# Kernel optimization log

Measured on AMD Instinct MI355X. Metric: run time of the kernel, lower is better.

Reference implementation:

```python
import jax, jax.numpy as jnp
import numpy as np

B, D, N = 256, 256, 100000
NUM_CLUSTERS, NUM_CLASSES = 100, 1000


def setup_inputs() -> dict:
    key = jax.random.key(0)
    k1, k2, k3, k4, k5, k6 = jax.random.split(key, 6)
    return {
        "feature": jax.random.normal(k1, (B, D), dtype=jnp.float32),
        "feature_bank": jax.random.normal(k2, (N, D), dtype=jnp.float32),
        "cluster_label_bank": jax.random.randint(k3, (N,), 0, NUM_CLUSTERS, dtype=jnp.int64)
            if jax.config.jax_enable_x64 else jax.random.randint(k3, (N,), 0, NUM_CLUSTERS).astype(jnp.int32),
        "class_label_bank": jax.random.randint(k4, (N,), 0, NUM_CLASSES).astype(jnp.int32),
        "cluster_idx": jax.random.randint(k5, (B,), 0, NUM_CLUSTERS).astype(jnp.int32),
        "gt_label": jax.random.randint(k6, (B,), 0, NUM_CLASSES).astype(jnp.int32),
    }


def reference(feature, feature_bank, cluster_label_bank, class_label_bank, cluster_idx, gt_label):
    # Masks: primary = same cluster AND different class; fallback = different class only.
    cluster_label_bank = cluster_label_bank.astype(jnp.int32)
    same_cluster = cluster_label_bank[None, :] == cluster_idx[:, None].astype(jnp.int32)  # [B, N]
    diff_class = class_label_bank[None, :] != gt_label[:, None]                            # [B, N]
    mask_primary = same_cluster & diff_class
    has_primary = mask_primary.any(axis=1, keepdims=True)
    mask = jnp.where(has_primary, mask_primary, diff_class)  # [B, N]

    # Euclidean distances (torch.cdist p=2): ||a-b|| via expanded squared form.
    a2 = jnp.sum(feature * feature, axis=1)[:, None]              # [B, 1]
    b2 = jnp.sum(feature_bank * feature_bank, axis=1)[None, :]    # [1, N]
    d2 = a2 + b2 - 2.0 * (feature @ feature_bank.T)               # [B, N]
    dist = jnp.sqrt(jnp.maximum(d2, 0.0))

    # Masked argmin over the bank, then gather negatives.
    dist_masked = jnp.where(mask, dist, jnp.inf)
    neg_idx = jnp.argmin(dist_masked, axis=1)                     # [B]
    negatives = feature_bank[neg_idx]                             # [B, D]
    return negatives
```

## Files before the change

### kernel.cpp

```cpp
#include <hip/hip_runtime.h>
#include <climits>

typedef __attribute__((ext_vector_type(8))) short s8;
typedef __attribute__((ext_vector_type(4))) float f32x4;

#define BQ    256
#define DDIM  256
#define NBANK 100000
#define BN    64
#define NJB   ((NBANK + BN - 1) / BN)
#define SENT  1e30f

__device__ inline void splitElem(float x, s8& h, s8& l, int i) {
    unsigned u  = __float_as_uint(x);
    unsigned uh = (u + 0x8000u) & 0xFFFF0000u;
    h[i] = (short)(uh >> 16);
    float lf = x - __uint_as_float(uh);
    l[i] = (short)((__float_as_uint(lf) + 0x8000u) >> 16);
}

__device__ inline void split8(const float4 v0, const float4 v1, s8& h, s8& l) {
    splitElem(v0.x, h, l, 0); splitElem(v0.y, h, l, 1);
    splitElem(v0.z, h, l, 2); splitElem(v0.w, h, l, 3);
    splitElem(v1.x, h, l, 4); splitElem(v1.y, h, l, 5);
    splitElem(v1.z, h, l, 6); splitElem(v1.w, h, l, 7);
}

__device__ inline float sq8(const float4 v0, const float4 v1, float s) {
    s = fmaf(v0.x, v0.x, s); s = fmaf(v0.y, v0.y, s);
    s = fmaf(v0.z, v0.z, s); s = fmaf(v0.w, v0.w, s);
    s = fmaf(v1.x, v1.x, s); s = fmaf(v1.y, v1.y, s);
    s = fmaf(v1.z, v1.z, s); s = fmaf(v1.w, v1.w, s);
    return s;
}

__global__ __launch_bounds__(512) void split_feature(
    const float* __restrict__ feature, s8* __restrict__ fH, s8* __restrict__ fL)
{
    const int t    = blockIdx.x * 512 + threadIdx.x;
    const int lane = t & 63, ks = (t >> 6) & 7, rt = t >> 9;
    const int row  = rt * 16 + (lane & 15);
    const int k0   = ks * 32 + (lane >> 4) * 8;
    const float* p = feature + (size_t)row * DDIM + k0;
    const float4 v0 = *(const float4*)p;
    const float4 v1 = *(const float4*)(p + 4);
    s8 h, l;
    split8(v0, v1, h, l);
    fH[t] = h; fL[t] = l;
}

__global__ __launch_bounds__(256, 3) void gemm_argmin_partial(
    const s8* __restrict__ fH, const s8* __restrict__ fL,
    const float* __restrict__ bank,
    const int* __restrict__ cluster_label, const int* __restrict__ class_label,
    const int* __restrict__ cluster_idx,  const int* __restrict__ gt_label,
    float* __restrict__ wsPV, int* __restrict__ wsPI,
    float* __restrict__ wsDV, int* __restrict__ wsDI)
{
    __shared__ __align__(16) s8 bHs[4 * 64];
    __shared__ __align__(16) s8 bLs[4 * 64];
    __shared__ float b2s[BN];
    __shared__ int clsS[BN], cluS[BN], rowGt[BQ], rowClu[BQ];

    const int tid = threadIdx.x;
    const int jb  = blockIdx.x;
    const int j0  = jb * BN;

    if (tid < BN) {
        int jg = j0 + tid;
        int jc = jg < NBANK ? jg : NBANK - 1;
        clsS[tid] = class_label[jc];
        cluS[tid] = cluster_label[jc];
    }
    rowGt[tid]  = gt_label[tid];
    rowClu[tid] = cluster_idx[tid];

    const int col = tid >> 2, q = tid & 3;
    const int ct_s = col >> 4, cl_s = col & 15;
    const int wi   = ct_s * 64 + q * 16 + cl_s;
    {
        int jcol = j0 + col;
        jcol = jcol < NBANK ? jcol : NBANK - 1;
        const float* gb = bank + (size_t)jcol * DDIM + q * 8;

        const int w = tid >> 6, lane = tid & 63;
        const int g = lane >> 4, c = lane & 15;

        f32x4 acc[4][4];
        #pragma unroll
        for (int ct = 0; ct < 4; ++ct)
            #pragma unroll
            for (int rt = 0; rt < 4; ++rt)
                acc[ct][rt] = (f32x4){0.f, 0.f, 0.f, 0.f};
        float sqa = 0.f;

        float4 cur0 = *(const float4*)(gb);
        float4 cur1 = *(const float4*)(gb + 4);

        for (int s = 0; s < 8; ++s) {
            s8 aHr[4], aLr[4];
            #pragma unroll
            for (int rt = 0; rt < 4; ++rt) {
                const int RT = w * 4 + rt;
                aHr[rt] = fH[(RT * 8 + s) * 64 + lane];
                aLr[rt] = fL[(RT * 8 + s) * 64 + lane];
            }
            __syncthreads();
            {
                s8 h, l;
                split8(cur0, cur1, h, l);
                sqa = sq8(cur0, cur1, sqa);
                bHs[wi] = h;
                bLs[wi] = l;
            }
            __syncthreads();
            if (s < 7) {
                cur0 = *(const float4*)(gb + (s + 1) * 32);
                cur1 = *(const float4*)(gb + (s + 1) * 32 + 4);
            }
            #pragma unroll
            for (int ct = 0; ct < 4; ++ct) {
                const s8 bh = bHs[ct * 64 + lane];
                const s8 bl = bLs[ct * 64 + lane];
                #pragma unroll
                for (int rt = 0; rt < 4; ++rt) {
                    acc[ct][rt] = __builtin_amdgcn_mfma_f32_16x16x32_bf16(aHr[rt], bh, acc[ct][rt], 0, 0, 0);
                    acc[ct][rt] = __builtin_amdgcn_mfma_f32_16x16x32_bf16(aHr[rt], bl, acc[ct][rt], 0, 0, 0);
                    acc[ct][rt] = __builtin_amdgcn_mfma_f32_16x16x32_bf16(aLr[rt], bh, acc[ct][rt], 0, 0, 0);
                    acc[ct][rt] = __builtin_amdgcn_mfma_f32_16x16x32_bf16(aLr[rt], bl, acc[ct][rt], 0, 0, 0);
                }
            }
        }

        sqa += __shfl_xor(sqa, 1);
        sqa += __shfl_xor(sqa, 2);
        if (q == 0) b2s[col] = sqa;
        __syncthreads();

        #pragma unroll
        for (int rt = 0; rt < 4; ++rt) {
            #pragma unroll
            for (int r = 0; r < 4; ++r) {
                const int row  = w * 64 + rt * 16 + g * 4 + r;
                const int myGt = rowGt[row], myClu = rowClu[row];
                float bpv = SENT, bdv = SENT;
                int   bpi = INT_MAX, bdi = INT_MAX;
                #pragma unroll
                for (int ct = 0; ct < 4; ++ct) {
                    const int jg = j0 + ct * 16 + c;
                    const float sc = b2s[ct * 16 + c] - 2.f * acc[ct][rt][r];
                    if (jg < NBANK && clsS[ct * 16 + c] != myGt) {
                        if (sc < bdv) { bdv = sc; bdi = jg; }
                        if (cluS[ct * 16 + c] == myClu && sc < bpv) { bpv = sc; bpi = jg; }
                    }
                }
                #pragma unroll
                for (int off = 1; off < 16; off <<= 1) {
                    float vv = __shfl_xor(bpv, off); int ii = __shfl_xor(bpi, off);
                    if (vv < bpv || (vv == bpv && ii < bpi)) { bpv = vv; bpi = ii; }
                    vv = __shfl_xor(bdv, off); ii = __shfl_xor(bdi, off);
                    if (vv < bdv || (vv == bdv && ii < bdi)) { bdv = vv; bdi = ii; }
                }
                if (c == 0) {
                    const size_t o = (size_t)row * NJB + jb;
                    wsPV[o] = bpv; wsPI[o] = bpi;
                    wsDV[o] = bdv; wsDI[o] = bdi;
                }
            }
        }
    }
}

__global__ __launch_bounds__(256) void reduce_gather(
    const float* __restrict__ wsPV, const int* __restrict__ wsPI,
    const float* __restrict__ wsDV, const int* __restrict__ wsDI,
    const float* __restrict__ bank, float* __restrict__ out)
{
    const int row = blockIdx.x, tid = threadIdx.x;
    float bpv = SENT, bdv = SENT;
    int   bpi = INT_MAX, bdi = INT_MAX;
    for (int b = tid; b < NJB; b += 256) {
        float v = wsPV[(size_t)row * NJB + b]; int ix = wsPI[(size_t)row * NJB + b];
        if (v < bpv || (v == bpv && ix < bpi)) { bpv = v; bpi = ix; }
        v = wsDV[(size_t)row * NJB + b]; ix = wsDI[(size_t)row * NJB + b];
        if (v < bdv || (v == bdv && ix < bdi)) { bdv = v; bdi = ix; }
    }
    #pragma unroll
    for (int off = 32; off > 0; off >>= 1) {
        float v = __shfl_down(bpv, off); int ix = __shfl_down(bpi, off);
        if (v < bpv || (v == bpv && ix < bpi)) { bpv = v; bpi = ix; }
        v = __shfl_down(bdv, off); ix = __shfl_down(bdi, off);
        if (v < bdv || (v == bdv && ix < bdi)) { bdv = v; bdi = ix; }
    }
    __shared__ float swPV[4], swDV[4];
    __shared__ int   swPI[4], swDI[4];
    __shared__ int   sIdx;
    const int lane = tid & 63, wv = tid >> 6;
    if (lane == 0) { swPV[wv] = bpv; swPI[wv] = bpi; swDV[wv] = bdv; swDI[wv] = bdi; }
    __syncthreads();
    if (tid == 0) {
        float pv = swPV[0]; int pi = swPI[0];
        float dv = swDV[0]; int di = swDI[0];
        #pragma unroll
        for (int w = 1; w < 4; ++w) {
            if (swPV[w] < pv || (swPV[w] == pv && swPI[w] < pi)) { pv = swPV[w]; pi = swPI[w]; }
            if (swDV[w] < dv || (swDV[w] == dv && swDI[w] < di)) { dv = swDV[w]; di = swDI[w]; }
        }
        sIdx = (pi != INT_MAX) ? pi : ((di != INT_MAX) ? di : 0);
    }
    __syncthreads();
    out[row * DDIM + tid] = bank[(size_t)sIdx * DDIM + tid];
}

extern "C" void kernel_launch(void* const* d_in, const int* in_sizes, int n_in,
                              void* d_out, int out_size, void* d_ws, size_t ws_size,
                              hipStream_t stream) {
    const float* feature       = (const float*)d_in[0];
    const float* bank          = (const float*)d_in[1];
    const int*   cluster_label = (const int*)d_in[2];
    const int*   class_label   = (const int*)d_in[3];
    const int*   cluster_idx   = (const int*)d_in[4];
    const int*   gt_label      = (const int*)d_in[5];
    float* out = (float*)d_out;

    s8* fH = (s8*)d_ws;
    s8* fL = fH + 8192;
    float* base = (float*)((char*)d_ws + 2 * 8192 * sizeof(s8));
    const size_t per = (size_t)BQ * NJB;
    float* wsPV = base;
    int*   wsPI = (int*)base + per;
    float* wsDV = base + 2 * per;
    int*   wsDI = (int*)base + 3 * per;

    hipLaunchKernelGGL(split_feature, dim3(16), dim3(512), 0, stream, feature, fH, fL);
    hipLaunchKernelGGL(gemm_argmin_partial, dim3(NJB), dim3(256), 0, stream,
                       fH, fL, bank, cluster_label, class_label, cluster_idx, gt_label,
                       wsPV, wsPI, wsDV, wsDI);
    hipLaunchKernelGGL(reduce_gather, dim3(BQ), dim3(256), 0, stream,
                       wsPV, wsPI, wsDV, wsDI, bank, out);
}
```

Before: 244.7 us.

## Stage full-K bank tile in shared memory and transpose partial workspace layout

Each block now loads its whole 64x256 bank tile into registers up front, splits it into bf16 hi/lo parts and writes them all to shared memory, then runs the full K loop of MFMAs with no per-step barriers. This removes the 16 __syncthreads of the old software-pipelined loop and lets all global loads be in flight at once. The partial-result workspace is transposed to block-major so the per-block stores are contiguous and the reduction reads are strided. Occupancy hint drops from 3 to 2 blocks per CU and shared memory grows to 64KB, which may reduce latency hiding.

```diff
diff --git a/kernel.cpp b/kernel.cpp
--- a/kernel.cpp
+++ b/kernel.cpp
@@ -49,7 +49,7 @@
     fH[t] = h; fL[t] = l;
 }
 
-__global__ __launch_bounds__(256, 3) void gemm_argmin_partial(
+__global__ __launch_bounds__(256, 2) void gemm_argmin_fullk(
     const s8* __restrict__ fH, const s8* __restrict__ fL,
     const float* __restrict__ bank,
     const int* __restrict__ cluster_label, const int* __restrict__ class_label,
@@ -57,8 +57,8 @@
     float* __restrict__ wsPV, int* __restrict__ wsPI,
     float* __restrict__ wsDV, int* __restrict__ wsDI)
 {
-    __shared__ __align__(16) s8 bHs[4 * 64];
-    __shared__ __align__(16) s8 bLs[4 * 64];
+    __shared__ __align__(16) s8 bHs[8 * 4 * 64];
+    __shared__ __align__(16) s8 bLs[8 * 4 * 64];
     __shared__ float b2s[BN];
     __shared__ int clsS[BN], cluS[BN], rowGt[BQ], rowClu[BQ];
 
@@ -77,95 +77,91 @@
 
     const int col = tid >> 2, q = tid & 3;
     const int ct_s = col >> 4, cl_s = col & 15;
-    const int wi   = ct_s * 64 + q * 16 + cl_s;
-    {
-        int jcol = j0 + col;
-        jcol = jcol < NBANK ? jcol : NBANK - 1;
-        const float* gb = bank + (size_t)jcol * DDIM + q * 8;
-
-        const int w = tid >> 6, lane = tid & 63;
-        const int g = lane >> 4, c = lane & 15;
-
-        f32x4 acc[4][4];
-        #pragma unroll
-        for (int ct = 0; ct < 4; ++ct)
-            #pragma unroll
-            for (int rt = 0; rt < 4; ++rt)
-                acc[ct][rt] = (f32x4){0.f, 0.f, 0.f, 0.f};
-        float sqa = 0.f;
-
-        float4 cur0 = *(const float4*)(gb);
-        float4 cur1 = *(const float4*)(gb + 4);
-
-        for (int s = 0; s < 8; ++s) {
-            s8 aHr[4], aLr[4];
+    int jcol = j0 + col; jcol = jcol < NBANK ? jcol : NBANK - 1;
+    const float* gb = bank + (size_t)jcol * DDIM + q * 8;
+
+    float4 v0[8], v1[8];
+    #pragma unroll
+    for (int s = 0; s < 8; ++s) {
+        v0[s] = *(const float4*)(gb + s * 32);
+        v1[s] = *(const float4*)(gb + s * 32 + 4);
+    }
+    float sqa = 0.f;
+    #pragma unroll
+    for (int s = 0; s < 8; ++s) {
+        s8 h, l;
+        split8(v0[s], v1[s], h, l);
+        sqa = sq8(v0[s], v1[s], sqa);
+        const int wi = (s * 4 + ct_s) * 64 + q * 16 + cl_s;
+        bHs[wi] = h;
+        bLs[wi] = l;
+    }
+    sqa += __shfl_xor(sqa, 1);
+    sqa += __shfl_xor(sqa, 2);
+    if (q == 0) b2s[col] = sqa;
+    __syncthreads();
+
+    const int w = tid >> 6, lane = tid & 63;
+    const int g = lane >> 4, c = lane & 15;
+
+    f32x4 acc[4][4];
+    #pragma unroll
+    for (int ct = 0; ct < 4; ++ct)
+        #pragma unroll
+        for (int rt = 0; rt < 4; ++rt)
+            acc[ct][rt] = (f32x4){0.f, 0.f, 0.f, 0.f};
+
+    #pragma unroll
+    for (int s = 0; s < 8; ++s) {
+        s8 aH[4], aL[4];
+        #pragma unroll
+        for (int rt = 0; rt < 4; ++rt) {
+            const int RT = w * 4 + rt;
+            aH[rt] = fH[(RT * 8 + s) * 64 + lane];
+            aL[rt] = fL[(RT * 8 + s) * 64 + lane];
+        }
+        #pragma unroll
+        for (int ct = 0; ct < 4; ++ct) {
+            const s8 bh = bHs[(s * 4 + ct) * 64 + lane];
+            const s8 bl = bLs[(s * 4 + ct) * 64 + lane];
             #pragma unroll
             for (int rt = 0; rt < 4; ++rt) {
-                const int RT = w * 4 + rt;
-                aHr[rt] = fH[(RT * 8 + s) * 64 + lane];
-                aLr[rt] = fL[(RT * 8 + s) * 64 + lane];
-            }
-            __syncthreads();
-            {
-                s8 h, l;
-                split8(cur0, cur1, h, l);
-                sqa = sq8(cur0, cur1, sqa);
-                bHs[wi] = h;
-                bLs[wi] = l;
-            }
-            __syncthreads();
-            if (s < 7) {
-                cur0 = *(const float4*)(gb + (s + 1) * 32);
-                cur1 = *(const float4*)(gb + (s + 1) * 32 + 4);
-            }
+                acc[ct][rt] = __builtin_amdgcn_mfma_f32_16x16x32_bf16(aH[rt], bh, acc[ct][rt], 0, 0, 0);
+                acc[ct][rt] = __builtin_amdgcn_mfma_f32_16x16x32_bf16(aH[rt], bl, acc[ct][rt], 0, 0, 0);
+                acc[ct][rt] = __builtin_amdgcn_mfma_f32_16x16x32_bf16(aL[rt], bh, acc[ct][rt], 0, 0, 0);
+                acc[ct][rt] = __builtin_amdgcn_mfma_f32_16x16x32_bf16(aL[rt], bl, acc[ct][rt], 0, 0, 0);
+            }
+        }
+    }
+
+    #pragma unroll
+    for (int rt = 0; rt < 4; ++rt) {
+        #pragma unroll
+        for (int r = 0; r < 4; ++r) {
+            const int row  = w * 64 + rt * 16 + g * 4 + r;
+            const int myGt = rowGt[row], myClu = rowClu[row];
+            float bpv = SENT, bdv = SENT;
+            int   bpi = INT_MAX, bdi = INT_MAX;
             #pragma unroll
             for (int ct = 0; ct < 4; ++ct) {
-                const s8 bh = bHs[ct * 64 + lane];
-                const s8 bl = bLs[ct * 64 + lane];
-                #pragma unroll
-                for (int rt = 0; rt < 4; ++rt) {
-                    acc[ct][rt] = __builtin_amdgcn_mfma_f32_16x16x32_bf16(aHr[rt], bh, acc[ct][rt], 0, 0, 0);
-                    acc[ct][rt] = __builtin_amdgcn_mfma_f32_16x16x32_bf16(aHr[rt], bl, acc[ct][rt], 0, 0, 0);
-                    acc[ct][rt] = __builtin_amdgcn_mfma_f32_16x16x32_bf16(aLr[rt], bh, acc[ct][rt], 0, 0, 0);
-                    acc[ct][rt] = __builtin_amdgcn_mfma_f32_16x16x32_bf16(aLr[rt], bl, acc[ct][rt], 0, 0, 0);
+                const int jg = j0 + ct * 16 + c;
+                const float sc = b2s[ct * 16 + c] - 2.f * acc[ct][rt][r];
+                if (jg < NBANK && clsS[ct * 16 + c] != myGt) {
+                    if (sc < bdv) { bdv = sc; bdi = jg; }
+                    if (cluS[ct * 16 + c] == myClu && sc < bpv) { bpv = sc; bpi = jg; }
                 }
             }
-        }
-
-        sqa += __shfl_xor(sqa, 1);
-        sqa += __shfl_xor(sqa, 2);
-        if (q == 0) b2s[col] = sqa;
-        __syncthreads();
-
-        #pragma unroll
-        for (int rt = 0; rt < 4; ++rt) {
             #pragma unroll
-            for (int r = 0; r < 4; ++r) {
-                const int row  = w * 64 + rt * 16 + g * 4 + r;
-                const int myGt = rowGt[row], myClu = rowClu[row];
-                float bpv = SENT, bdv = SENT;
-                int   bpi = INT_MAX, bdi = INT_MAX;
-                #pragma unroll
-                for (int ct = 0; ct < 4; ++ct) {
-                    const int jg = j0 + ct * 16 + c;
-                    const float sc = b2s[ct * 16 + c] - 2.f * acc[ct][rt][r];
-                    if (jg < NBANK && clsS[ct * 16 + c] != myGt) {
-                        if (sc < bdv) { bdv = sc; bdi = jg; }
-                        if (cluS[ct * 16 + c] == myClu && sc < bpv) { bpv = sc; bpi = jg; }
-                    }
-                }
-                #pragma unroll
-                for (int off = 1; off < 16; off <<= 1) {
-                    float vv = __shfl_xor(bpv, off); int ii = __shfl_xor(bpi, off);
-                    if (vv < bpv || (vv == bpv && ii < bpi)) { bpv = vv; bpi = ii; }
-                    vv = __shfl_xor(bdv, off); ii = __shfl_xor(bdi, off);
-                    if (vv < bdv || (vv == bdv && ii < bdi)) { bdv = vv; bdi = ii; }
-                }
-                if (c == 0) {
-                    const size_t o = (size_t)row * NJB + jb;
-                    wsPV[o] = bpv; wsPI[o] = bpi;
-                    wsDV[o] = bdv; wsDI[o] = bdi;
-                }
+            for (int off = 1; off < 16; off <<= 1) {
+                float vv = __shfl_xor(bpv, off); int ii = __shfl_xor(bpi, off);
+                if (vv < bpv || (vv == bpv && ii < bpi)) { bpv = vv; bpi = ii; }
+                vv = __shfl_xor(bdv, off); ii = __shfl_xor(bdi, off);
+                if (vv < bdv || (vv == bdv && ii < bdi)) { bdv = vv; bdi = ii; }
+            }
+            if (c == 0) {
+                const size_t o = (size_t)jb * BQ + row;
+                wsPV[o] = bpv; wsPI[o] = bpi;
+                wsDV[o] = bdv; wsDI[o] = bdi;
             }
         }
     }
@@ -180,9 +176,10 @@
     float bpv = SENT, bdv = SENT;
     int   bpi = INT_MAX, bdi = INT_MAX;
     for (int b = tid; b < NJB; b += 256) {
-        float v = wsPV[(size_t)row * NJB + b]; int ix = wsPI[(size_t)row * NJB + b];
+        const size_t o = (size_t)b * BQ + row;
+        float v = wsPV[o]; int ix = wsPI[o];
         if (v < bpv || (v == bpv && ix < bpi)) { bpv = v; bpi = ix; }
-        v = wsDV[(size_t)row * NJB + b]; ix = wsDI[(size_t)row * NJB + b];
+        v = wsDV[o]; ix = wsDI[o];
         if (v < bdv || (v == bdv && ix < bdi)) { bdv = v; bdi = ix; }
     }
     #pragma unroll
@@ -233,7 +230,7 @@
     int*   wsDI = (int*)base + 3 * per;
 
     hipLaunchKernelGGL(split_feature, dim3(16), dim3(512), 0, stream, feature, fH, fL);
-    hipLaunchKernelGGL(gemm_argmin_partial, dim3(NJB), dim3(256), 0, stream,
+    hipLaunchKernelGGL(gemm_argmin_fullk, dim3(NJB), dim3(256), 0, stream,
                        fH, fL, bank, cluster_label, class_label, cluster_idx, gt_label,
                        wsPV, wsPI, wsDV, wsDI);
     hipLaunchKernelGGL(reduce_gather, dim3(BQ), dim3(256), 0, stream,
```

New measurement: 273.1 us. +11.6%, slower.
